# Optimization experiments

Measured on AMD Instinct MI355X. Metric: run time of the kernel, lower is better.

## Reference

```python
import jax, jax.numpy as jnp
import numpy as np

TOPK = 2  # matches init_kwargs topk


def setup_inputs() -> dict:
    key = jax.random.key(0)
    k1, k2 = jax.random.split(key)
    T, D, E = 32768, 4096, 16
    hidden_states = jax.random.normal(k1, (T, D), dtype=jnp.float32)
    wg_weight = jax.random.normal(k2, (E, D), dtype=jnp.float32) * 0.02  # [num_experts, hidden]
    return {"hidden_states": hidden_states, "wg_weight": wg_weight}


def reference(hidden_states, wg_weight):
    # logits = hidden_states @ wg.T  -> [T, E], computed in fp32 as in the torch module
    logits = jnp.einsum("td,ed->te", hidden_states.astype(jnp.float32), wg_weight.astype(jnp.float32))
    gates = jax.nn.softmax(logits, axis=-1)  # [T, E]
    topk_weights, topk_indices = jax.lax.top_k(gates, TOPK)  # [T, K] each
    topk_weights = topk_weights / jnp.sum(topk_weights, axis=-1, keepdims=True)
    return topk_indices, topk_weights.astype(hidden_states.dtype)
```

## Files before the change

### kernel.cpp

```cpp
#include <hip/hip_runtime.h>
#include <math.h>

#define T_TOKENS 32768
#define HID      4096
#define NEXP     16
#define MT       8
#define WAVES    8
#define D4       (HID / 4)
#define HALF     (D4 / 2)
#define NC       (HALF / 64)

typedef float f32x4 __attribute__((ext_vector_type(4)));

__global__ __launch_bounds__(512, 2) void moe_gate_kernel(
    const float* __restrict__ h,
    const float* __restrict__ w,
    float* __restrict__ out)
{
    __shared__ f32x4 sw[NEXP][HALF];

    const int lane = threadIdx.x & 63;
    const int wv   = threadIdx.x >> 6;
    const int t0   = blockIdx.x * (MT * WAVES) + wv * MT;

    const f32x4* __restrict__ w4 = reinterpret_cast<const f32x4*>(w);
    const f32x4* hrow[MT];
    #pragma unroll
    for (int t = 0; t < MT; ++t)
        hrow[t] = reinterpret_cast<const f32x4*>(h + (size_t)(t0 + t) * HID);

    float acc[MT * NEXP];
    #pragma unroll
    for (int i = 0; i < MT * NEXP; ++i) acc[i] = 0.0f;

#define STAGE(kh_) do {                                                       \
        _Pragma("unroll")                                                     \
        for (int j = 0; j < 16; ++j) {                                        \
            const int e_ = 2 * wv + (j >> 3);                                 \
            const int c_ = j & 7;                                             \
            const f32x4* gsrc =                                               \
                w4 + (size_t)e_ * D4 + (kh_) * HALF + c_ * 64 + lane;         \
            __builtin_amdgcn_global_load_lds(                                 \
                (const __attribute__((address_space(1))) void*)gsrc,          \
                (__attribute__((address_space(3))) void*)&sw[e_][c_ * 64],    \
                16, 0, 0);                                                    \
        }                                                                     \
    } while (0)

#define LOADH(dst, kh_, c_) do {                                              \
        const int d4_ = (kh_) * HALF + (c_) * 64 + lane;                      \
        _Pragma("unroll")                                                     \
        for (int t = 0; t < MT; ++t)                                          \
            dst[t] = __builtin_nontemporal_load(&hrow[t][d4_]);               \
    } while (0)

#define COMPUTE(c_, hreg) do {                                                \
        _Pragma("unroll")                                                     \
        for (int e_ = 0; e_ < NEXP; ++e_) {                                   \
            f32x4 wvv = sw[e_][(c_) * 64 + lane];                             \
            _Pragma("unroll")                                                 \
            for (int t = 0; t < MT; ++t) {                                    \
                float a = acc[t * NEXP + e_];                                 \
                a = fmaf(hreg[t][0], wvv[0], a);                              \
                a = fmaf(hreg[t][1], wvv[1], a);                              \
                a = fmaf(hreg[t][2], wvv[2], a);                              \
                a = fmaf(hreg[t][3], wvv[3], a);                              \
                acc[t * NEXP + e_] = a;                                       \
            }                                                                 \
        }                                                                     \
    } while (0)

    f32x4 hv[MT], hn[MT];

    for (int kh = 0; kh < 2; ++kh) {
        if (kh) {
            asm volatile("s_waitcnt lgkmcnt(0)" ::: "memory");
            __builtin_amdgcn_s_barrier();
            asm volatile("" ::: "memory");
        }
        STAGE(kh);
        __builtin_amdgcn_sched_barrier(0);
        LOADH(hv, kh, 0);
        asm volatile("s_waitcnt vmcnt(8)" ::: "memory");
        __builtin_amdgcn_s_barrier();
        asm volatile("" ::: "memory");
        __builtin_amdgcn_sched_barrier(0);

        #pragma unroll 1
        for (int c = 0; c < NC - 1; ++c) {
            LOADH(hn, kh, c + 1);
            COMPUTE(c, hv);
            #pragma unroll
            for (int t = 0; t < MT; ++t) hv[t] = hn[t];
        }
        COMPUTE(NC - 1, hv);
    }

#define BUTTERFLY(base) do {                                                  \
        _Pragma("unroll")                                                     \
        for (int b = 32; b >= 1; b >>= 1) {                                   \
            const bool hi_ = (lane & b) != 0;                                 \
            _Pragma("unroll")                                                 \
            for (int j = 0; j < b; ++j) {                                     \
                float lo_v = acc[(base) + j];                                 \
                float hi_v = acc[(base) + j + b];                             \
                float keepv = hi_ ? hi_v : lo_v;                              \
                float sendv = hi_ ? lo_v : hi_v;                              \
                acc[(base) + j] = keepv + __shfl_xor(sendv, b, 64);           \
            }                                                                 \
        }                                                                     \
    } while (0)

    BUTTERFLY(0);
    BUTTERFLY(64);
    const float logit0 = acc[0];
    const float logit1 = acc[64];

    const int eidx = lane & 15;
#define TOP2_WRITE(logit_, tok_) do {                                         \
        float m1 = (logit_); int i1 = eidx;                                   \
        _Pragma("unroll")                                                     \
        for (int s = 1; s < 16; s <<= 1) {                                    \
            float ov = __shfl_xor(m1, s, 64);                                 \
            int   oi = __shfl_xor(i1, s, 64);                                 \
            if (ov > m1 || (ov == m1 && oi < i1)) { m1 = ov; i1 = oi; }       \
        }                                                                     \
        float masked = (eidx == i1) ? -INFINITY : (logit_);                   \
        float m2 = masked; int i2 = eidx;                                     \
        _Pragma("unroll")                                                     \
        for (int s = 1; s < 16; s <<= 1) {                                    \
            float ov = __shfl_xor(m2, s, 64);                                 \
            int   oi = __shfl_xor(i2, s, 64);                                 \
            if (ov > m2 || (ov == m2 && oi < i2)) { m2 = ov; i2 = oi; }       \
        }                                                                     \
        if (eidx == 0) {                                                      \
            const float r_ = expf(m2 - m1);                                   \
            const float s_ = 1.0f / (1.0f + r_);                              \
            float2* oidx = reinterpret_cast<float2*>(out);                    \
            float2* owt  = reinterpret_cast<float2*>(out + 2 * T_TOKENS);     \
            oidx[tok_] = make_float2((float)i1, (float)i2);                   \
            owt[tok_]  = make_float2(s_, r_ * s_);                            \
        }                                                                     \
    } while (0)

    TOP2_WRITE(logit0, t0 + (lane >> 4));
    TOP2_WRITE(logit1, t0 + 4 + (lane >> 4));

#undef STAGE
#undef LOADH
#undef COMPUTE
#undef BUTTERFLY
#undef TOP2_WRITE
}

extern "C" void kernel_launch(void* const* d_in, const int* in_sizes, int n_in,
                              void* d_out, int out_size, void* d_ws, size_t ws_size,
                              hipStream_t stream) {
    const float* h = (const float*)d_in[0];
    const float* w = (const float*)d_in[1];
    float* out = (float*)d_out;

    const int blocks = T_TOKENS / (MT * WAVES);
    moe_gate_kernel<<<blocks, 512, 0, stream>>>(h, w, out);
}
```

Baseline: 112.9 us.

## Triple-buffer hidden-state loads and overlap second-half prefetch with weight restage

Replaces the double-buffered per-chunk hidden-state loads with a three-buffer rotation so global loads run two chunks ahead, removing the register copy between buffers. The first chunks of the second K-half are prefetched before the LDS weight restage, so restaging overlaps with in-flight loads. Row pointers are collapsed into one wave-uniform base pointer. The extra buffer raises VGPR pressure under the existing launch bounds, which risks spills.

```diff
diff --git a/kernel.cpp b/kernel.cpp
--- a/kernel.cpp
+++ b/kernel.cpp
@@ -2,8 +2,8 @@
 #include <math.h>
 
 #define T_TOKENS 32768
+#define NEXP     16
 #define HID      4096
-#define NEXP     16
 #define MT       8
 #define WAVES    8
 #define D4       (HID / 4)
@@ -22,12 +22,10 @@
     const int lane = threadIdx.x & 63;
     const int wv   = threadIdx.x >> 6;
     const int t0   = blockIdx.x * (MT * WAVES) + wv * MT;
-
+    const int t0u  = __builtin_amdgcn_readfirstlane(t0);
+    const f32x4* __restrict__ hb =
+        reinterpret_cast<const f32x4*>(h + (size_t)t0u * HID);
     const f32x4* __restrict__ w4 = reinterpret_cast<const f32x4*>(w);
-    const f32x4* hrow[MT];
-    #pragma unroll
-    for (int t = 0; t < MT; ++t)
-        hrow[t] = reinterpret_cast<const f32x4*>(h + (size_t)(t0 + t) * HID);
 
     float acc[MT * NEXP];
     #pragma unroll
@@ -47,11 +45,11 @@
         }                                                                     \
     } while (0)
 
-#define LOADH(dst, kh_, c_) do {                                              \
-        const int d4_ = (kh_) * HALF + (c_) * 64 + lane;                      \
+#define LOADH(dst, g_) do {                                                   \
+        const int d4_ = (g_) * 64 + lane;                                     \
         _Pragma("unroll")                                                     \
         for (int t = 0; t < MT; ++t)                                          \
-            dst[t] = __builtin_nontemporal_load(&hrow[t][d4_]);               \
+            dst[t] = __builtin_nontemporal_load(hb + (size_t)t * D4 + d4_);   \
     } while (0)
 
 #define COMPUTE(c_, hreg) do {                                                \
@@ -70,31 +68,45 @@
         }                                                                     \
     } while (0)
 
-    f32x4 hv[MT], hn[MT];
+#define PHASELOOP(A, B, C, kb_) do {                                          \
+        _Pragma("unroll 1")                                                   \
+        for (int c = 0; c < NC - 2; c += 3) {                                 \
+            LOADH(C, (kb_) + c + 2); COMPUTE(c + 0, A);                       \
+            LOADH(A, (kb_) + c + 3); COMPUTE(c + 1, B);                       \
+            LOADH(B, (kb_) + c + 4); COMPUTE(c + 2, C);                       \
+        }                                                                     \
+    } while (0)
 
-    for (int kh = 0; kh < 2; ++kh) {
-        if (kh) {
-            asm volatile("s_waitcnt lgkmcnt(0)" ::: "memory");
-            __builtin_amdgcn_s_barrier();
-            asm volatile("" ::: "memory");
-        }
-        STAGE(kh);
-        __builtin_amdgcn_sched_barrier(0);
-        LOADH(hv, kh, 0);
-        asm volatile("s_waitcnt vmcnt(8)" ::: "memory");
-        __builtin_amdgcn_s_barrier();
-        asm volatile("" ::: "memory");
-        __builtin_amdgcn_sched_barrier(0);
+    f32x4 hv, hn, h2;
+    f32x4 bA[MT], bB[MT], bC[MT];
+    (void)hv; (void)hn; (void)h2;
 
-        #pragma unroll 1
-        for (int c = 0; c < NC - 1; ++c) {
-            LOADH(hn, kh, c + 1);
-            COMPUTE(c, hv);
-            #pragma unroll
-            for (int t = 0; t < MT; ++t) hv[t] = hn[t];
-        }
-        COMPUTE(NC - 1, hv);
-    }
+    STAGE(0);
+    __builtin_amdgcn_sched_barrier(0);
+    LOADH(bA, 0);
+    LOADH(bB, 1);
+    asm volatile("s_waitcnt vmcnt(16)" ::: "memory");
+    __builtin_amdgcn_s_barrier();
+    asm volatile("" ::: "memory");
+    __builtin_amdgcn_sched_barrier(0);
+
+    PHASELOOP(bA, bB, bC, 0);
+    LOADH(bC, 8); COMPUTE(NC - 2, bA);
+    LOADH(bA, 9); COMPUTE(NC - 1, bB);
+
+    asm volatile("s_waitcnt lgkmcnt(0)" ::: "memory");
+    __builtin_amdgcn_s_barrier();
+    asm volatile("" ::: "memory");
+    STAGE(1);
+    __builtin_amdgcn_sched_barrier(0);
+    asm volatile("s_waitcnt vmcnt(0)" ::: "memory");
+    __builtin_amdgcn_s_barrier();
+    asm volatile("" ::: "memory");
+    __builtin_amdgcn_sched_barrier(0);
+
+    PHASELOOP(bC, bA, bB, NC);
+    COMPUTE(NC - 2, bC);
+    COMPUTE(NC - 1, bA);
 
 #define BUTTERFLY(base) do {                                                  \
         _Pragma("unroll")                                                     \
@@ -149,6 +161,7 @@
 #undef STAGE
 #undef LOADH
 #undef COMPUTE
+#undef PHASELOOP
 #undef BUTTERFLY
 #undef TOP2_WRITE
 }
```

Result: slower. 255.9 us (+126.7%).
